# Kernel optimization log

Measured on AMD Instinct MI355X. Metric: run time of the kernel, lower is better.

Reference implementation:

```python
import jax, jax.numpy as jnp
import numpy as np

RANK = 4
ALPHA = 4.0
SCALE = ALPHA / RANK


def setup_inputs() -> dict:
    key = jax.random.key(0)
    k1, k2, k3, k4 = jax.random.split(key, 4)
    B, S, H = 4, 2048, 2048
    NH, HD = 16, 128
    x = jax.random.normal(k1, (B, S, H), dtype=jnp.float32)
    W_orig = jax.random.normal(k2, (H, NH, HD), dtype=jnp.float32) * (1.0 / np.sqrt(H))
    A_kernel = jax.random.normal(k3, (H, RANK), dtype=jnp.float32) * (1.0 / RANK)
    # B kernel is zero-init in the module; use small randn so the LoRA path is exercised
    B_kernel = jax.random.normal(k4, (RANK, NH, HD), dtype=jnp.float32) * 0.02
    return {"x": x, "W_orig": W_orig, "A_kernel": A_kernel, "B_kernel": B_kernel}


def reference(x, W_orig, A_kernel, B_kernel):
    # original layer: EinsumDense 'abc,cde->abde'  [B,S,H] x [H,NH,HD] -> [B,S,NH,HD]
    original_output = jnp.einsum('bsc,chd->bshd', x, W_orig)
    # LoRA path: Dense to rank, then EinsumDense back up, scaled
    ax = x @ A_kernel                                   # [B,S,r]
    lora_output = jnp.einsum('bsr,rhd->bshd', ax, B_kernel) * SCALE
    return original_output + lora_output
```

## Files before the change

kernel.cpp:

```cpp
#include <hip/hip_runtime.h>
#include <hip/hip_bf16.h>
#include <cstdint>


using bf16 = __hip_bfloat16;
typedef __attribute__((ext_vector_type(8))) __bf16 bf16x8;
typedef __attribute__((ext_vector_type(4))) float f32x4;

constexpr int Mdim = 8192;
constexpr int Ndim = 2048;
constexpr int Kdim = 2048;
constexpr float SCALE = 1.0f;

constexpr int BM = 256, BN = 256, BK = 64;
constexpr int NT2 = Kdim / (2 * BK);
constexpr int CVT_BLOCKS = (Mdim * Kdim) / (256 * 8);
constexpr int PREP_BLOCKS = (Ndim / 64) * (Kdim / 64);

__device__ __forceinline__ void gload_lds16(const void* g, void* l) {
  __builtin_amdgcn_global_load_lds(
      (const __attribute__((address_space(1))) uint32_t*)g,
      (__attribute__((address_space(3))) uint32_t*)l,
      16, 0, 0);
}

__global__ void prep_all(const float* __restrict__ X,
                         const float* __restrict__ W,
                         const float* __restrict__ A,
                         const float* __restrict__ Bk,
                         uint16_t* __restrict__ Xb,
                         uint16_t* __restrict__ Wt) {
  __shared__ float tile[64][65];

  if (blockIdx.x < CVT_BLOCKS) {
    const int i = blockIdx.x * blockDim.x + threadIdx.x;
    const float4* Xv = (const float4*)X;
    float4 a = Xv[i * 2 + 0];
    float4 b = Xv[i * 2 + 1];
    uint16_t o[8];
    o[0] = __bfloat16_as_ushort(__float2bfloat16(a.x));
    o[1] = __bfloat16_as_ushort(__float2bfloat16(a.y));
    o[2] = __bfloat16_as_ushort(__float2bfloat16(a.z));
    o[3] = __bfloat16_as_ushort(__float2bfloat16(a.w));
    o[4] = __bfloat16_as_ushort(__float2bfloat16(b.x));
    o[5] = __bfloat16_as_ushort(__float2bfloat16(b.y));
    o[6] = __bfloat16_as_ushort(__float2bfloat16(b.z));
    o[7] = __bfloat16_as_ushort(__float2bfloat16(b.w));
    *reinterpret_cast<uint4*>(Xb + (size_t)i * 8) = *reinterpret_cast<uint4*>(o);
  } else {
    const int pid = blockIdx.x - CVT_BLOCKS;
    const int tx = threadIdx.x & 63;
    const int ty = threadIdx.x >> 6;
    const int n0 = (pid & 31) * 64, k0 = (pid >> 5) * 64;

    const int n = n0 + tx;
    const float b0 = Bk[0 * Ndim + n];
    const float b1 = Bk[1 * Ndim + n];
    const float b2 = Bk[2 * Ndim + n];
    const float b3 = Bk[3 * Ndim + n];

    for (int i = ty; i < 64; i += 4) {
      const int k = k0 + i;
      float w = W[(size_t)k * Ndim + n];
      w += SCALE * (A[k * 4 + 0] * b0 + A[k * 4 + 1] * b1 +
                    A[k * 4 + 2] * b2 + A[k * 4 + 3] * b3);
      tile[tx][i] = w;
    }
    __syncthreads();
    for (int i = ty; i < 64; i += 4) {
      Wt[(size_t)(n0 + i) * Kdim + (k0 + tx)] =
          __bfloat16_as_ushort(__float2bfloat16(tile[i][tx]));
    }
  }
}

#define FENCE() asm volatile("" ::: "memory")
#define VMW(N)  asm volatile("s_waitcnt vmcnt(" #N ")" ::: "memory")
#define PH()                                                                   \
  do {                                                                         \
    FENCE();                                                                   \
    __builtin_amdgcn_s_barrier();                                              \
    FENCE();                                                                   \
  } while (0)

__global__ __launch_bounds__(512, 2) void gemm_8ph(
    const uint16_t* __restrict__ X, const uint16_t* __restrict__ Wt,
    float* __restrict__ out) {
  __shared__ uint16_t lds[65536];

  const int t = threadIdx.x;
  const int wave = t >> 6, lane = t & 63;
  const int wm = wave >> 2, wn = wave & 3;
  const int l15 = lane & 15, kg = lane >> 4;
  const int sw = l15 & 7;

  const int lid = blockIdx.x;
  const int xcd = lid & 7, loc = lid >> 3;
  const int by = xcd * 4 + (loc & 3);
  const int bx = loc >> 2;
  const int m0 = by * BM, n0 = bx * BN;

  const uint16_t* Ag = X + (size_t)m0 * Kdim;
  const uint16_t* Bg = Wt + (size_t)n0 * Kdim;

  const int r8 = lane >> 3;
  const int gc = (lane & 7) ^ r8;
  const int slot0 = wave * 2, slot1 = slot0 + 1;
  const size_t go0 = (size_t)(slot0 * 8 + r8) * Kdim + gc * 8;
  const size_t go1 = (size_t)(slot1 * 8 + r8) * Kdim + gc * 8;

  int aE[2], bE[2];
#pragma unroll
  for (int s2 = 0; s2 < 2; ++s2) {
    const int p = (s2 * 4 + kg) ^ sw;
    aE[s2] = (wm * 64 + l15) * 64 + p * 8;
    bE[s2] = (wn * 32 + l15) * 64 + p * 8;
  }

#define STAGE_A(buf, h, kt)                                                    \
  do {                                                                         \
    gload_lds16(Ag + go0 + (size_t)(h) * 128 * Kdim + (kt),                    \
                &lds[(buf) * 32768 + (h) * 8192 + slot0 * 512]);               \
    gload_lds16(Ag + go1 + (size_t)(h) * 128 * Kdim + (kt),                    \
                &lds[(buf) * 32768 + (h) * 8192 + slot1 * 512]);               \
  } while (0)
#define STAGE_B(buf, h, kt)                                                    \
  do {                                                                         \
    gload_lds16(Bg + go0 + (size_t)(h) * 128 * Kdim + (kt),                    \
                &lds[(buf) * 32768 + 16384 + (h) * 8192 + slot0 * 512]);       \
    gload_lds16(Bg + go1 + (size_t)(h) * 128 * Kdim + (kt),                    \
                &lds[(buf) * 32768 + 16384 + (h) * 8192 + slot1 * 512]);       \
  } while (0)

  bf16x8 a[4][2], b0[2][2], b1[2][2];
  f32x4 acc[8][4] = {};

#define READ_A(QM, buf)                                                        \
  do {                                                                         \
    _Pragma("unroll") for (int ii = 0; ii < 4; ++ii)                           \
        _Pragma("unroll") for (int s2 = 0; s2 < 2; ++s2)                       \
            a[ii][s2] = *reinterpret_cast<const bf16x8*>(                      \
                &lds[(buf) * 32768 + (QM) * 8192 + ii * 1024 + aE[s2]]);       \
  } while (0)
#define READ_B(QN, buf, dst)                                                   \
  do {                                                                         \
    _Pragma("unroll") for (int jj = 0; jj < 2; ++jj)                           \
        _Pragma("unroll") for (int s2 = 0; s2 < 2; ++s2)                       \
            dst[jj][s2] = *reinterpret_cast<const bf16x8*>(                    \
                &lds[(buf) * 32768 + 16384 + (QN) * 8192 + jj * 1024 +         \
                     bE[s2]]);                                                 \
  } while (0)
#define MMA(QM, QN, barr)                                                      \
  do {                                                                         \
    __builtin_amdgcn_s_setprio(1);                                             \
    _Pragma("unroll") for (int s2 = 0; s2 < 2; ++s2)                           \
        _Pragma("unroll") for (int ii = 0; ii < 4; ++ii)                       \
            _Pragma("unroll") for (int jj = 0; jj < 2; ++jj)                   \
                acc[(QM) * 4 + ii][(QN) * 2 + jj] =                            \
                    __builtin_amdgcn_mfma_f32_16x16x32_bf16(                   \
                        a[ii][s2], barr[jj][s2],                               \
                        acc[(QM) * 4 + ii][(QN) * 2 + jj], 0, 0, 0);           \
    __builtin_amdgcn_s_setprio(0);                                             \
    __builtin_amdgcn_sched_barrier(0);                                         \
  } while (0)
#define STORE_Q(QM, QN)                                                        \
  do {                                                                         \
    _Pragma("unroll") for (int ii = 0; ii < 4; ++ii) {                         \
      const int mb = m0 + (QM) * 128 + wm * 64 + ii * 16 + kg * 4;             \
      _Pragma("unroll") for (int jj = 0; jj < 2; ++jj) {                       \
        const int n = n0 + (QN) * 128 + wn * 32 + jj * 16 + l15;               \
        _Pragma("unroll") for (int r = 0; r < 4; ++r)                          \
            out[(size_t)(mb + r) * Ndim + n] =                                 \
                acc[(QM) * 4 + ii][(QN) * 2 + jj][r];                          \
      }                                                                        \
    }                                                                          \
  } while (0)

  STAGE_B(0, 0, 0); STAGE_A(0, 0, 0); STAGE_B(0, 1, 0); STAGE_A(0, 1, 0);
  FENCE();
  STAGE_B(1, 0, BK); STAGE_A(1, 0, BK); STAGE_B(1, 1, BK);
  FENCE();
  VMW(6); PH();
  READ_A(0, 0); READ_B(0, 0, b0);
  STAGE_A(1, 1, BK);

#pragma unroll 1
  for (int j = 0; j < NT2 - 1; ++j) {
    const int kn0 = j * 128 + 128;
    const int kn1 = j * 128 + 192;

    PH(); MMA(0, 0, b0); READ_B(1, 0, b1);
    PH(); MMA(0, 1, b1); READ_A(1, 0); STAGE_B(0, 0, kn0);
    PH(); MMA(1, 1, b1); STAGE_A(0, 0, kn0);
    VMW(6); PH(); MMA(1, 0, b0);
    READ_A(0, 1); READ_B(0, 1, b0); STAGE_B(0, 1, kn0);
    PH(); MMA(0, 0, b0); READ_B(1, 1, b1); STAGE_A(0, 1, kn0);
    VMW(8); PH(); MMA(0, 1, b1);
    READ_A(1, 1); STAGE_B(1, 0, kn1); STAGE_A(1, 0, kn1);
    PH(); MMA(1, 1, b1); STAGE_B(1, 1, kn1);
    VMW(6); PH(); MMA(1, 0, b0);
    READ_A(0, 0); READ_B(0, 0, b0); STAGE_A(1, 1, kn1);
  }

  PH(); MMA(0, 0, b0); READ_B(1, 0, b1);
  PH(); MMA(0, 1, b1); READ_A(1, 0);
  PH(); MMA(1, 1, b1);
  VMW(4); PH(); MMA(1, 0, b0); READ_A(0, 1); READ_B(0, 1, b0);
  VMW(0); PH(); MMA(0, 0, b0); READ_B(1, 1, b1); STORE_Q(0, 0);
  PH(); MMA(0, 1, b1); READ_A(1, 1); STORE_Q(0, 1);
  PH(); MMA(1, 1, b1); STORE_Q(1, 1);
  PH(); MMA(1, 0, b0); STORE_Q(1, 0);

#undef STAGE_A
#undef STAGE_B
#undef READ_A
#undef READ_B
#undef MMA
#undef STORE_Q
}

extern "C" void kernel_launch(void* const* d_in, const int* in_sizes, int n_in,
                              void* d_out, int out_size, void* d_ws, size_t ws_size,
                              hipStream_t stream) {
  const float* x  = (const float*)d_in[0];
  const float* W  = (const float*)d_in[1];
  const float* A  = (const float*)d_in[2];
  const float* Bk = (const float*)d_in[3];
  float* out = (float*)d_out;

  uint16_t* Xb = (uint16_t*)d_ws;
  uint16_t* Wt = (uint16_t*)((char*)d_ws + (size_t)Mdim * Kdim * 2);

  prep_all<<<CVT_BLOCKS + PREP_BLOCKS, 256, 0, stream>>>(x, W, A, Bk, Xb, Wt);

  gemm_8ph<<<(Mdim / BM) * (Ndim / BN), 512, 0, stream>>>(Xb, Wt, out);
}
```

Before: 191.2 us.

## Fuse prep and GEMM into one cooperative kernel with grid sync

Merges the bf16 conversion of X, the LoRA weight merge and transpose, and the GEMM into a single cooperative launch of 256 blocks, separated by a grid-wide barrier. Each block now converts a strided share of X and four 64x64 weight tiles before the sync. The aim is to remove the second kernel launch and the gap between the two kernels. In exchange the prep work runs on only 256 blocks of 512 threads rather than many small blocks, and the grid sync adds its own cost. It also removes the sched_barrier after each MFMA group, keeps the two-kernel path as a fallback, and adds an unused lgkmcnt wait macro.

```diff
diff --git a/kernel.cpp b/kernel.cpp
--- a/kernel.cpp
+++ b/kernel.cpp
@@ -1,7 +1,10 @@
 #include <hip/hip_runtime.h>
 #include <hip/hip_bf16.h>
+#include <hip/hip_cooperative_groups.h>
 #include <cstdint>
 
+
+namespace cg = cooperative_groups;
 
 using bf16 = __hip_bfloat16;
 typedef __attribute__((ext_vector_type(8))) __bf16 bf16x8;
@@ -24,58 +27,13 @@
       16, 0, 0);
 }
 
-__global__ void prep_all(const float* __restrict__ X,
-                         const float* __restrict__ W,
-                         const float* __restrict__ A,
-                         const float* __restrict__ Bk,
-                         uint16_t* __restrict__ Xb,
-                         uint16_t* __restrict__ Wt) {
-  __shared__ float tile[64][65];
-
-  if (blockIdx.x < CVT_BLOCKS) {
-    const int i = blockIdx.x * blockDim.x + threadIdx.x;
-    const float4* Xv = (const float4*)X;
-    float4 a = Xv[i * 2 + 0];
-    float4 b = Xv[i * 2 + 1];
-    uint16_t o[8];
-    o[0] = __bfloat16_as_ushort(__float2bfloat16(a.x));
-    o[1] = __bfloat16_as_ushort(__float2bfloat16(a.y));
-    o[2] = __bfloat16_as_ushort(__float2bfloat16(a.z));
-    o[3] = __bfloat16_as_ushort(__float2bfloat16(a.w));
-    o[4] = __bfloat16_as_ushort(__float2bfloat16(b.x));
-    o[5] = __bfloat16_as_ushort(__float2bfloat16(b.y));
-    o[6] = __bfloat16_as_ushort(__float2bfloat16(b.z));
-    o[7] = __bfloat16_as_ushort(__float2bfloat16(b.w));
-    *reinterpret_cast<uint4*>(Xb + (size_t)i * 8) = *reinterpret_cast<uint4*>(o);
-  } else {
-    const int pid = blockIdx.x - CVT_BLOCKS;
-    const int tx = threadIdx.x & 63;
-    const int ty = threadIdx.x >> 6;
-    const int n0 = (pid & 31) * 64, k0 = (pid >> 5) * 64;
-
-    const int n = n0 + tx;
-    const float b0 = Bk[0 * Ndim + n];
-    const float b1 = Bk[1 * Ndim + n];
-    const float b2 = Bk[2 * Ndim + n];
-    const float b3 = Bk[3 * Ndim + n];
-
-    for (int i = ty; i < 64; i += 4) {
-      const int k = k0 + i;
-      float w = W[(size_t)k * Ndim + n];
-      w += SCALE * (A[k * 4 + 0] * b0 + A[k * 4 + 1] * b1 +
-                    A[k * 4 + 2] * b2 + A[k * 4 + 3] * b3);
-      tile[tx][i] = w;
-    }
-    __syncthreads();
-    for (int i = ty; i < 64; i += 4) {
-      Wt[(size_t)(n0 + i) * Kdim + (k0 + tx)] =
-          __bfloat16_as_ushort(__float2bfloat16(tile[i][tx]));
-    }
-  }
+__device__ __forceinline__ uint16_t f2bf(float f) {
+  return __bfloat16_as_ushort(__float2bfloat16(f));
 }
 
 #define FENCE() asm volatile("" ::: "memory")
 #define VMW(N)  asm volatile("s_waitcnt vmcnt(" #N ")" ::: "memory")
+#define LGKM8() asm volatile("s_waitcnt lgkmcnt(8)" ::: "memory")
 #define PH()                                                                   \
   do {                                                                         \
     FENCE();                                                                   \
@@ -83,11 +41,10 @@
     FENCE();                                                                   \
   } while (0)
 
-__global__ __launch_bounds__(512, 2) void gemm_8ph(
-    const uint16_t* __restrict__ X, const uint16_t* __restrict__ Wt,
-    float* __restrict__ out) {
-  __shared__ uint16_t lds[65536];
-
+__device__ __forceinline__ void gemm_body(const uint16_t* __restrict__ X,
+                                          const uint16_t* __restrict__ Wt,
+                                          float* __restrict__ out,
+                                          uint16_t* lds) {
   const int t = threadIdx.x;
   const int wave = t >> 6, lane = t & 63;
   const int wm = wave >> 2, wn = wave & 3;
@@ -161,7 +118,6 @@
                         a[ii][s2], barr[jj][s2],                               \
                         acc[(QM) * 4 + ii][(QN) * 2 + jj], 0, 0, 0);           \
     __builtin_amdgcn_s_setprio(0);                                             \
-    __builtin_amdgcn_sched_barrier(0);                                         \
   } while (0)
 #define STORE_Q(QM, QN)                                                        \
   do {                                                                         \
@@ -219,6 +175,118 @@
 #undef STORE_Q
 }
 
+__device__ __forceinline__ void prep_body_fused(const float* __restrict__ X,
+                                                const float* __restrict__ W,
+                                                const float* __restrict__ A,
+                                                const float* __restrict__ Bk,
+                                                uint16_t* __restrict__ Xb,
+                                                uint16_t* __restrict__ Wt,
+                                                uint16_t* lds) {
+  const int t = threadIdx.x;
+  const int b = blockIdx.x;
+
+  {
+    const float4* Xv = (const float4*)X;
+#pragma unroll 4
+    for (int it = 0; it < 16; ++it) {
+      const int u = b * 512 + t + it * (256 * 512);
+      float4 a4 = Xv[u * 2 + 0];
+      float4 b4 = Xv[u * 2 + 1];
+      uint16_t o[8];
+      o[0] = f2bf(a4.x); o[1] = f2bf(a4.y); o[2] = f2bf(a4.z); o[3] = f2bf(a4.w);
+      o[4] = f2bf(b4.x); o[5] = f2bf(b4.y); o[6] = f2bf(b4.z); o[7] = f2bf(b4.w);
+      *reinterpret_cast<uint4*>(Xb + (size_t)u * 8) = *reinterpret_cast<uint4*>(o);
+    }
+  }
+
+  float* tile = (float*)lds;
+  const int tx = t & 63;
+  const int ty = t >> 6;
+  for (int tt = 0; tt < 4; ++tt) {
+    const int pid = b * 4 + tt;
+    const int n0 = (pid & 31) * 64, k0 = (pid >> 5) * 64;
+    const int n = n0 + tx;
+    const float c0 = Bk[0 * Ndim + n];
+    const float c1 = Bk[1 * Ndim + n];
+    const float c2 = Bk[2 * Ndim + n];
+    const float c3 = Bk[3 * Ndim + n];
+    __syncthreads();
+#pragma unroll
+    for (int i = ty; i < 64; i += 8) {
+      const int k = k0 + i;
+      float w = W[(size_t)k * Ndim + n];
+      w += SCALE * (A[k * 4 + 0] * c0 + A[k * 4 + 1] * c1 +
+                    A[k * 4 + 2] * c2 + A[k * 4 + 3] * c3);
+      tile[tx * 65 + i] = w;
+    }
+    __syncthreads();
+#pragma unroll
+    for (int i = ty; i < 64; i += 8) {
+      Wt[(size_t)(n0 + i) * Kdim + (k0 + tx)] = f2bf(tile[i * 65 + tx]);
+    }
+  }
+}
+
+__global__ __launch_bounds__(512, 2) void fused_all(
+    const float* __restrict__ X, const float* __restrict__ W,
+    const float* __restrict__ A, const float* __restrict__ Bk,
+    uint16_t* __restrict__ Xb, uint16_t* __restrict__ Wt,
+    float* __restrict__ out) {
+  __shared__ uint16_t lds[65536];
+  prep_body_fused(X, W, A, Bk, Xb, Wt, lds);
+  __threadfence();
+  cg::this_grid().sync();
+  gemm_body(Xb, Wt, out, lds);
+}
+
+__global__ void prep_all(const float* __restrict__ X,
+                         const float* __restrict__ W,
+                         const float* __restrict__ A,
+                         const float* __restrict__ Bk,
+                         uint16_t* __restrict__ Xb,
+                         uint16_t* __restrict__ Wt) {
+  __shared__ float tile[64][65];
+
+  if (blockIdx.x < CVT_BLOCKS) {
+    const int i = blockIdx.x * blockDim.x + threadIdx.x;
+    const float4* Xv = (const float4*)X;
+    float4 a = Xv[i * 2 + 0];
+    float4 b = Xv[i * 2 + 1];
+    uint16_t o[8];
+    o[0] = f2bf(a.x); o[1] = f2bf(a.y); o[2] = f2bf(a.z); o[3] = f2bf(a.w);
+    o[4] = f2bf(b.x); o[5] = f2bf(b.y); o[6] = f2bf(b.z); o[7] = f2bf(b.w);
+    *reinterpret_cast<uint4*>(Xb + (size_t)i * 8) = *reinterpret_cast<uint4*>(o);
+  } else {
+    const int pid = blockIdx.x - CVT_BLOCKS;
+    const int tx = threadIdx.x & 63;
+    const int ty = threadIdx.x >> 6;
+    const int n0 = (pid & 31) * 64, k0 = (pid >> 5) * 64;
+    const int n = n0 + tx;
+    const float b0 = Bk[0 * Ndim + n];
+    const float b1 = Bk[1 * Ndim + n];
+    const float b2 = Bk[2 * Ndim + n];
+    const float b3 = Bk[3 * Ndim + n];
+    for (int i = ty; i < 64; i += 4) {
+      const int k = k0 + i;
+      float w = W[(size_t)k * Ndim + n];
+      w += SCALE * (A[k * 4 + 0] * b0 + A[k * 4 + 1] * b1 +
+                    A[k * 4 + 2] * b2 + A[k * 4 + 3] * b3);
+      tile[tx][i] = w;
+    }
+    __syncthreads();
+    for (int i = ty; i < 64; i += 4) {
+      Wt[(size_t)(n0 + i) * Kdim + (k0 + tx)] = f2bf(tile[i][tx]);
+    }
+  }
+}
+
+__global__ __launch_bounds__(512, 2) void gemm_8ph(
+    const uint16_t* __restrict__ X, const uint16_t* __restrict__ Wt,
+    float* __restrict__ out) {
+  __shared__ uint16_t lds[65536];
+  gemm_body(X, Wt, out, lds);
+}
+
 extern "C" void kernel_launch(void* const* d_in, const int* in_sizes, int n_in,
                               void* d_out, int out_size, void* d_ws, size_t ws_size,
                               hipStream_t stream) {
@@ -231,7 +299,28 @@
   uint16_t* Xb = (uint16_t*)d_ws;
   uint16_t* Wt = (uint16_t*)((char*)d_ws + (size_t)Mdim * Kdim * 2);
 
-  prep_all<<<CVT_BLOCKS + PREP_BLOCKS, 256, 0, stream>>>(x, W, A, Bk, Xb, Wt);
-
-  gemm_8ph<<<(Mdim / BM) * (Ndim / BN), 512, 0, stream>>>(Xb, Wt, out);
-}
+  static int coop_checked = 0, coop_ok = 0;
+  if (!coop_checked) {
+    int dev = 0;
+    (void)hipGetDevice(&dev);
+    int v = 0;
+    if (hipDeviceGetAttribute(&v, hipDeviceAttributeCooperativeLaunch, dev) ==
+        hipSuccess)
+      coop_ok = v;
+    coop_checked = 1;
+  }
+
+  bool launched = false;
+  if (coop_ok) {
+    void* args[] = {(void*)&x, (void*)&W, (void*)&A, (void*)&Bk,
+                    (void*)&Xb, (void*)&Wt, (void*)&out};
+    hipError_t e = hipLaunchCooperativeKernel(
+        reinterpret_cast<void*>(fused_all), dim3(256), dim3(512), args, 0,
+        stream);
+    launched = (e == hipSuccess);
+  }
+  if (!launched) {
+    prep_all<<<CVT_BLOCKS + PREP_BLOCKS, 256, 0, stream>>>(x, W, A, Bk, Xb, Wt);
+    gemm_8ph<<<(Mdim / BM) * (Ndim / BN), 512, 0, stream>>>(Xb, Wt, out);
+  }
+}
```

New measurement: 276.5 us. +44.6%, slower.
